# Kernel tuning notes

Measured on AMD Instinct MI355X. Metric: run time of the kernel, lower is better.

The kernel has to match this reference:

```python
import jax, jax.numpy as jnp
import numpy as np
from jax import lax

VOCAB = 50000
EMB = 300
HID = 256
N = 4096          # total_sents
T_COL = 64
T_ROW = 16
N_DOCS = 512


def setup_inputs() -> dict:
    key = jax.random.key(0)
    ks = jax.random.split(key, 20)

    def glorot(k, shape):
        fan = float(sum(shape))
        return (jax.random.normal(k, shape, jnp.float32) * (2.0 / fan) ** 0.5)

    inp = {}
    inp["col"] = jax.random.randint(ks[0], (N, T_COL), 0, VOCAB, dtype=jnp.int32)
    inp["row"] = jax.random.randint(ks[1], (N, T_ROW), 0, VOCAB, dtype=jnp.int32)
    inp["row_neg"] = jax.random.randint(ks[2], (N, T_ROW), 0, VOCAB, dtype=jnp.int32)
    # pack_padded_sequence expects lengths sorted descending
    inp["col_lens"] = jnp.sort(jax.random.randint(ks[3], (N,), 1, T_COL + 1, dtype=jnp.int32))[::-1]
    inp["row_lens"] = jnp.sort(jax.random.randint(ks[4], (N,), 1, T_ROW + 1, dtype=jnp.int32))[::-1]
    inp["row_neg_lens"] = jnp.sort(jax.random.randint(ks[5], (N,), 1, T_ROW + 1, dtype=jnp.int32))[::-1]
    inp["col_refs"] = jax.random.randint(ks[6], (N,), 0, N_DOCS, dtype=jnp.int32)
    inp["row_refs"] = jax.random.randint(ks[7], (N,), 0, N_DOCS, dtype=jnp.int32)
    inp["row_neg_refs"] = jax.random.randint(ks[8], (N,), 0, N_DOCS, dtype=jnp.int32)
    inp["embed_table"] = jax.random.normal(ks[9], (VOCAB, EMB), jnp.float32) * 0.1
    inp["col_W_ih"] = glorot(ks[10], (4 * HID, EMB))
    inp["col_W_hh"] = glorot(ks[11], (4 * HID, HID))
    inp["col_b_ih"] = jnp.zeros((4 * HID,), jnp.float32)
    inp["col_b_hh"] = jnp.zeros((4 * HID,), jnp.float32)
    inp["row_W_ih"] = glorot(ks[12], (4 * HID, EMB))
    inp["row_W_hh"] = glorot(ks[13], (4 * HID, HID))
    inp["row_b_ih"] = jnp.zeros((4 * HID,), jnp.float32)
    inp["row_b_hh"] = jnp.zeros((4 * HID,), jnp.float32)
    return inp


def lstm_last_hidden(x, lengths, W_ih, W_hh, b_ih, b_hh):
    """x: [N,T,E]; returns hidden state at step lengths-1 per sequence: [N,H].
    Equivalent to torch LSTM over a packed padded sequence (state frozen past len)."""
    Nn, T, _ = x.shape
    H = W_hh.shape[1]
    h0 = jnp.zeros((Nn, H), x.dtype)
    bias = b_ih + b_hh

    def step(carry, inputs):
        h, c = carry
        xt, t = inputs  # xt: [N,E]
        gates = xt @ W_ih.T + h @ W_hh.T + bias  # [N,4H]
        i, f, g, o = jnp.split(gates, 4, axis=-1)  # torch gate order i,f,g,o
        i = jax.nn.sigmoid(i); f = jax.nn.sigmoid(f); o = jax.nn.sigmoid(o)
        g = jnp.tanh(g)
        c_new = f * c + i * g
        h_new = o * jnp.tanh(c_new)
        m = (t < lengths)[:, None]
        return (jnp.where(m, h_new, h), jnp.where(m, c_new, c)), None

    (h, _), _ = lax.scan(step, (h0, h0), (jnp.swapaxes(x, 0, 1), jnp.arange(T)))
    return h


def reference(col, row, row_neg, col_lens, row_lens, row_neg_lens,
              col_refs, row_refs, row_neg_refs, embed_table,
              col_W_ih, col_W_hh, col_b_ih, col_b_hh,
              row_W_ih, row_W_hh, row_b_ih, row_b_hh):
    # Dropout is identity (eval-mode reference).
    def compose(tokens, lens, refs, W_ih, W_hh, b_ih, b_hh):
        emb = embed_table[tokens]                      # [N,T,E]
        h = lstm_last_hidden(emb, lens, W_ih, W_hh, b_ih, b_hh)  # [N,H]
        # mask-multiply + sum == segment-sum of hidden states by doc ref,
        # scattered into a [total_sents, H] buffer (rows >= n_docs are zero)
        return jax.ops.segment_sum(h, refs, num_segments=tokens.shape[0])

    col_h = compose(col, col_lens, col_refs, col_W_ih, col_W_hh, col_b_ih, col_b_hh)
    row_h = compose(row, row_lens, row_refs, row_W_ih, row_W_hh, row_b_ih, row_b_hh)
    neg_h = compose(row_neg, row_neg_lens, row_neg_refs, row_W_ih, row_W_hh, row_b_ih, row_b_hh)

    pos = jnp.sum(col_h * row_h, axis=1)
    neg = jnp.sum(col_h * neg_h, axis=1)
    # BPRLoss(size_average=False): sum of -logsigmoid(pos - neg)
    return -jnp.sum(jax.nn.log_sigmoid(pos - neg))
```

## Files before the change

kernel.cpp:

```cpp
#include <hip/hip_runtime.h>


typedef __bf16 bf16x8 __attribute__((ext_vector_type(8)));
typedef float  fvec4  __attribute__((ext_vector_type(4)));

#define NSEN 4096
#define HIDN 256
#define EMBD 300
#define VOC  50000

#define OFF_P     0ULL
#define OFF_BPK   204800000ULL
#define OFF_WHHC  206110720ULL
#define OFF_WHHR  206635008ULL
#define OFF_BIAS  207159296ULL
#define OFF_SEG   219750400ULL
#define OFF_LOSS  232333312ULL

static __device__ __forceinline__ unsigned short f2bf(float x) {
    unsigned int u = __float_as_uint(x);
    unsigned int r = (u + 0x7fffu + ((u >> 16) & 1u)) >> 16;
    return (unsigned short)r;
}
static __device__ __forceinline__ float bf2f(unsigned short b) {
    return __uint_as_float(((unsigned int)b) << 16);
}
static __device__ __forceinline__ float sigm(float x) { return 1.f / (1.f + __expf(-x)); }
static __device__ __forceinline__ float tanh_(float x) {
    float e = __expf(2.f * x);
    return 1.f - 2.f / (e + 1.f);
}
static __device__ __forceinline__ fvec4 unpk(uint2 v) {
    fvec4 o;
    o[0] = __uint_as_float((v.x & 0xffffu) << 16);
    o[1] = __uint_as_float(v.x & 0xffff0000u);
    o[2] = __uint_as_float((v.y & 0xffffu) << 16);
    o[3] = __uint_as_float(v.y & 0xffff0000u);
    return o;
}

static __device__ __forceinline__ void gld_lds16(const unsigned short* g,
                                                 unsigned short* l)
{
    __builtin_amdgcn_global_load_lds(
        (const __attribute__((address_space(1))) unsigned int*)g,
        (__attribute__((address_space(3))) unsigned int*)l, 16, 0, 0);
}

static __device__ __forceinline__ int whh_src(int o) {
    int L  = o >> 9;
    int r9 = o & 511;
    int ln = r9 >> 3, j = r9 & 7;
    int g  = L & 3, kt = (L >> 2) & 7, wv = (L >> 5) & 15;
    int row = g * 256 + wv * 16 + (ln & 15);
    int col = kt * 32 + (ln >> 4) * 8 + j;
    return row * 256 + col;
}

__global__ void prep_kernel(
    const float* __restrict__ cWih, const float* __restrict__ rWih,
    const float* __restrict__ cWhh, const float* __restrict__ rWhh,
    const float* __restrict__ cbih, const float* __restrict__ cbhh,
    const float* __restrict__ rbih, const float* __restrict__ rbhh,
    unsigned short* __restrict__ Bpk, unsigned short* __restrict__ WhhC,
    unsigned short* __restrict__ WhhR, float* __restrict__ biascat)
{
    int idx = blockIdx.x * 256 + threadIdx.x;
    if (idx < 655360) {
        int e = idx & 511, lnn = e >> 3, j = e & 7;
        int f = idx >> 9;
        int ntt = f & 3;
        int kc = f >> 2;
        int kt = kc % 10;
        int s  = kc / 10;
        int n = (s >> 1) * 128 + (s & 1) * 64 + ntt * 16 + (lnn & 15);
        int k = kt * 32 + (lnn >> 4) * 8 + j;
        float v = 0.f;
        if (k < EMBD) v = (n < 1024) ? cWih[n * EMBD + k] : rWih[(n - 1024) * EMBD + k];
        Bpk[idx] = f2bf(v);
        return;
    }
    idx -= 655360;
    if (idx < 262144) { WhhC[idx] = f2bf(cWhh[whh_src(idx)]); return; }
    idx -= 262144;
    if (idx < 262144) { WhhR[idx] = f2bf(rWhh[whh_src(idx)]); return; }
    idx -= 262144;
    if (idx < 2048)
        biascat[idx] = (idx < 1024) ? (cbih[idx] + cbhh[idx])
                                    : (rbih[idx - 1024] + rbhh[idx - 1024]);
}

__global__ __launch_bounds__(256) void gemm_p_kernel(
    const float* __restrict__ A,
    const unsigned short* __restrict__ Bpk,
    const float* __restrict__ bias,
    unsigned short* __restrict__ Pout)
{
    const int mb = blockIdx.x * 128;
    const int tid = threadIdx.x;
    const int wv = tid >> 6, ln = tid & 63, l15 = ln & 15, q = ln >> 4;
    const int wm = wv & 1, wn = wv >> 1;

    __shared__ __align__(16) unsigned short At[2][4][10][512];

    {
        int row = tid >> 1, kh = tid & 1;
        int gr = mb + row;
        unsigned short* dst = &At[row >> 6][(row >> 4) & 3][0][0];
        const int fl = row & 15;
        #pragma unroll
        for (int i = 0; i < 40; ++i) {
            int k = kh * 160 + i * 4;
            float4 v = make_float4(0.f, 0.f, 0.f, 0.f);
            if (gr < VOC && k < EMBD)
                v = *(const float4*)(A + (size_t)gr * EMBD + k);
            ushort4 b;
            b.x = f2bf(v.x); b.y = f2bf(v.y); b.z = f2bf(v.z); b.w = f2bf(v.w);
            int di = (k >> 5) * 512 + ((k >> 3) & 3) * 128 + fl * 8 + (k & 7);
            *(ushort4*)(dst + di) = b;
        }
    }
    __syncthreads();

    for (int nc = 0; nc < 16; ++nc) {
        fvec4 acc[4][4];
        #pragma unroll
        for (int a = 0; a < 4; ++a)
            #pragma unroll
            for (int b = 0; b < 4; ++b) acc[a][b] = (fvec4)0.f;

        #pragma unroll 2
        for (int kt = 0; kt < 10; ++kt) {
            const unsigned short* bp =
                Bpk + (size_t)(((nc * 2 + wn) * 10 + kt) * 4) * 512 + ln * 8;
            bf16x8 bfr[4];
            #pragma unroll
            for (int ntt = 0; ntt < 4; ++ntt)
                bfr[ntt] = *(const bf16x8*)(bp + ntt * 512);
            #pragma unroll
            for (int mt = 0; mt < 4; ++mt) {
                bf16x8 af = *(const bf16x8*)&At[wm][mt][kt][ln * 8];
                #pragma unroll
                for (int ntt = 0; ntt < 4; ++ntt)
                    acc[mt][ntt] = __builtin_amdgcn_mfma_f32_16x16x32_bf16(
                        af, bfr[ntt], acc[mt][ntt], 0, 0, 0);
            }
        }
        float bv[4];
        #pragma unroll
        for (int ntt = 0; ntt < 4; ++ntt)
            bv[ntt] = bias[nc * 128 + wn * 64 + ntt * 16 + l15];
        #pragma unroll
        for (int mt = 0; mt < 4; ++mt) {
            #pragma unroll
            for (int r = 0; r < 4; ++r) {
                int m = mb + wm * 64 + mt * 16 + q * 4 + r;
                if (m < VOC) {
                    size_t base = (size_t)m * 2048 + nc * 128 + wn * 64;
                    #pragma unroll
                    for (int ntt = 0; ntt < 4; ++ntt)
                        Pout[base + ntt * 16 + l15] = f2bf(acc[mt][ntt][r] + bv[ntt]);
                }
            }
        }
    }
}

__global__ __launch_bounds__(1024, 2) void lstm_kernel(
    const int* __restrict__ colTok, const int* __restrict__ rowTok, const int* __restrict__ negTok,
    const int* __restrict__ colLen, const int* __restrict__ rowLen, const int* __restrict__ negLen,
    const int* __restrict__ crefs, const int* __restrict__ rrefs, const int* __restrict__ nrefs,
    const unsigned short* __restrict__ P,
    const unsigned short* __restrict__ WhhC, const unsigned short* __restrict__ WhhR,
    float* __restrict__ seg)
{
    const int part = blockIdx.x >> 8;
    const int sb = blockIdx.x & 255;
    const int s0 = sb * 16;
    const int* tok = part == 0 ? colTok : (part == 1 ? rowTok : negTok);
    const int* len = part == 0 ? colLen : (part == 1 ? rowLen : negLen);
    const int* refs = part == 0 ? crefs : (part == 1 ? rrefs : nrefs);
    const unsigned short* Whh = part == 0 ? WhhC : WhhR;
    const int T = part == 0 ? 64 : 16;
    const int pco = part == 0 ? 0 : 1024;
    float* segp = seg + (size_t)part * 1048576;

    const int tid = threadIdx.x;
    const int wv = tid >> 6;
    const int ln = tid & 63, l15 = ln & 15, q = ln >> 4;

    __shared__ __align__(16) unsigned short hx[2][8][4][16][8];
    __shared__ __align__(16) unsigned short pstage[2][16][4][2][16][8];
    __shared__ __align__(16) char ldspad[1536];
    char* hB0 = (char*)&hx[0][0][0][0][0];
    char* hB1 = (char*)&hx[1][0][0][0][0];

    for (int i = tid; i < 8192; i += 1024) (&hx[0][0][0][0][0])[i] = 0;

    const int len0 = len[s0 + l15];
    int ml = len0;
    #pragma unroll
    for (int off = 1; off < 16; off <<= 1) ml = max(ml, __shfl_xor(ml, off));
    const int maxlen = ml;
    if (maxlen < 0) ldspad[tid & 1023] = 1;

    const unsigned short* wbase = Whh + (size_t)wv * 16384 + (size_t)ln * 8;

    const int wrByte = (wv >> 1) * 1024 + ((wv & 1) * 2 + (q >> 1)) * 256 +
                       l15 * 16 + (q & 1) * 8;

    const int dg = ln >> 5, dh = (ln >> 4) & 1;

    float c[4];
    #pragma unroll
    for (int r = 0; r < 4; ++r) c[r] = 0.f;
    ushort4 hpk = make_ushort4(0, 0, 0, 0);

    __syncthreads();

    {
        int tk = tok[(s0 + l15) * T];
        #pragma unroll
        for (int d = 0; d < 2; ++d) {
            const unsigned short* src = P + (size_t)tk * 2048 + pco +
                (2 * d + dg) * 256 + wv * 16 + dh * 8;
            gld_lds16(src, &pstage[0][wv][2 * d][0][0][0]);
        }
    }
    int tknext = tok[(s0 + l15) * T + 1];

    for (int t = 0; t < maxlen; ++t) {
        const int pb = t & 1;
        const char* hRd = (t & 1) ? hB1 : hB0;
        char* hWr = (t & 1) ? hB0 : hB1;

        asm volatile("s_waitcnt vmcnt(0)" ::: "memory");

        fvec4 acc[4];
        #pragma unroll
        for (int g = 0; g < 4; ++g)
            acc[g] = unpk(*(const uint2*)
                &pstage[pb][wv][g][q >> 1][l15][(q & 1) * 4]);

        #pragma unroll 2
        for (int kt = 0; kt < 8; ++kt) {
            bf16x8 b0 = *(const bf16x8*)(hRd + kt * 1024 + ln * 16);
            #pragma unroll
            for (int g = 0; g < 4; ++g) {
                bf16x8 a = *(const bf16x8*)(wbase + (size_t)(kt * 4 + g) * 512);
                acc[g] = __builtin_amdgcn_mfma_f32_16x16x32_bf16(a, b0, acc[g], 0, 0, 0);
            }
        }

        if (t + 1 < maxlen) {
            __builtin_amdgcn_sched_barrier(0);
            #pragma unroll
            for (int d = 0; d < 2; ++d) {
                const unsigned short* src = P + (size_t)tknext * 2048 + pco +
                    (2 * d + dg) * 256 + wv * 16 + dh * 8;
                gld_lds16(src, &pstage[pb ^ 1][wv][2 * d][0][0][0]);
            }
            int t2 = (t + 2 < T) ? (t + 2) : (T - 1);
            tknext = tok[(s0 + l15) * T + t2];
        }

        {
            bool act = t < len0;
            if (act) {
                float hr[4];
                #pragma unroll
                for (int r = 0; r < 4; ++r) {
                    float iv = acc[0][r];
                    float fv = acc[1][r];
                    float gv = acc[2][r];
                    float ov = acc[3][r];
                    float cn = sigm(fv) * c[r] + sigm(iv) * tanh_(gv);
                    c[r] = cn;
                    hr[r] = sigm(ov) * tanh_(cn);
                }
                hpk = make_ushort4(f2bf(hr[0]), f2bf(hr[1]),
                                   f2bf(hr[2]), f2bf(hr[3]));
            }
            *(ushort4*)(hWr + wrByte) = hpk;
        }
        asm volatile("s_waitcnt lgkmcnt(0)\n\ts_barrier" ::: "memory");
    }

    const char* hF = (maxlen & 1) ? hB1 : hB0;
    for (int i = tid; i < 16 * HIDN; i += 1024) {
        int sq = i >> 8, hd = i & 255;
        unsigned short hv = *(const unsigned short*)
            (hF + (hd >> 5) * 1024 + ((hd >> 3) & 3) * 256 +
             sq * 16 + (hd & 7) * 2);
        int rf = refs[s0 + sq];
        atomicAdd(segp + (size_t)rf * 256 + hd, bf2f(hv));
    }
}

__global__ void loss_kernel(const float* __restrict__ seg, float* __restrict__ part)
{
    int d = blockIdx.x, tid = threadIdx.x;
    const float* sc = seg + (size_t)d * 256;
    const float* sr = seg + 1048576 + (size_t)d * 256;
    const float* sn = seg + 2097152 + (size_t)d * 256;
    float a = sc[tid];
    float p = a * sr[tid];
    float n = a * sn[tid];
    for (int off = 32; off; off >>= 1) { p += __shfl_down(p, off); n += __shfl_down(n, off); }
    __shared__ float rp[4], rn[4];
    if ((tid & 63) == 0) { rp[tid >> 6] = p; rn[tid >> 6] = n; }
    __syncthreads();
    if (tid == 0) {
        float Ps = rp[0] + rp[1] + rp[2] + rp[3];
        float Ns = rn[0] + rn[1] + rn[2] + rn[3];
        float x = Ps - Ns;
        part[d] = fmaxf(-x, 0.f) + log1pf(expf(-fabsf(x)));
    }
}

__global__ void reduce_kernel(const float* __restrict__ part, float* __restrict__ out)
{
    int tid = threadIdx.x;
    float s = 0.f;
    for (int i = tid; i < 4096; i += 256) s += part[i];
    for (int off = 32; off; off >>= 1) s += __shfl_down(s, off);
    __shared__ float r[4];
    if ((tid & 63) == 0) r[tid >> 6] = s;
    __syncthreads();
    if (tid == 0) out[0] = r[0] + r[1] + r[2] + r[3];
}

extern "C" void kernel_launch(void* const* d_in, const int* in_sizes, int n_in,
                              void* d_out, int out_size, void* d_ws, size_t ws_size,
                              hipStream_t stream)
{
    const int*   col      = (const int*)d_in[0];
    const int*   row      = (const int*)d_in[1];
    const int*   rneg     = (const int*)d_in[2];
    const int*   col_lens = (const int*)d_in[3];
    const int*   row_lens = (const int*)d_in[4];
    const int*   rng_lens = (const int*)d_in[5];
    const int*   col_refs = (const int*)d_in[6];
    const int*   row_refs = (const int*)d_in[7];
    const int*   rng_refs = (const int*)d_in[8];
    const float* embed    = (const float*)d_in[9];
    const float* cWih     = (const float*)d_in[10];
    const float* cWhh     = (const float*)d_in[11];
    const float* cbih     = (const float*)d_in[12];
    const float* cbhh     = (const float*)d_in[13];
    const float* rWih     = (const float*)d_in[14];
    const float* rWhh     = (const float*)d_in[15];
    const float* rbih     = (const float*)d_in[16];
    const float* rbhh     = (const float*)d_in[17];

    char* ws = (char*)d_ws;
    unsigned short* P    = (unsigned short*)(ws + OFF_P);
    unsigned short* Bpk  = (unsigned short*)(ws + OFF_BPK);
    unsigned short* WhhC = (unsigned short*)(ws + OFF_WHHC);
    unsigned short* WhhR = (unsigned short*)(ws + OFF_WHHR);
    float* biascat = (float*)(ws + OFF_BIAS);
    float* seg     = (float*)(ws + OFF_SEG);
    float* lpart   = (float*)(ws + OFF_LOSS);

    hipMemsetAsync(seg, 0, 3 * 4096 * 256 * sizeof(float), stream);

    prep_kernel<<<4616, 256, 0, stream>>>(cWih, rWih, cWhh, rWhh,
                                          cbih, cbhh, rbih, rbhh,
                                          Bpk, WhhC, WhhR, biascat);
    gemm_p_kernel<<<391, 256, 0, stream>>>(embed, Bpk, biascat, P);
    lstm_kernel<<<768, 1024, 0, stream>>>(col, row, rneg,
                                          col_lens, row_lens, rng_lens,
                                          col_refs, row_refs, rng_refs,
                                          P, WhhC, WhhR, seg);
    loss_kernel<<<4096, 256, 0, stream>>>(seg, lpart);
    reduce_kernel<<<1, 256, 0, stream>>>(lpart, (float*)d_out);
}
```

Baseline: 689.5 us.

## Keep half of W_hh in registers and single-buffer the input projection stage

Half of each wave's recurrent weight fragments (the first four k-tiles) are now loaded once into registers instead of being re-read from global memory every timestep. The staging buffer for precomputed input projections goes from double to single buffering, and the padding array that forced an LDS size limit is removed. The projection add moves after the MFMA loop, with a wait on the prefetch placed there, so the global load latency overlaps the matmul. This lowers per-step weight traffic and LDS use, which may allow more blocks per CU. The cost is 64 extra VGPRs per thread and a serialized prefetch within each step.

Result: faster. 601.4 us (-12.8%).

```diff
diff --git a/kernel.cpp b/kernel.cpp
--- a/kernel.cpp
+++ b/kernel.cpp
@@ -190,8 +190,7 @@
     const int ln = tid & 63, l15 = ln & 15, q = ln >> 4;
 
     __shared__ __align__(16) unsigned short hx[2][8][4][16][8];
-    __shared__ __align__(16) unsigned short pstage[2][16][4][2][16][8];
-    __shared__ __align__(16) char ldspad[1536];
+    __shared__ __align__(16) unsigned short pstage[16][4][2][16][8];
     char* hB0 = (char*)&hx[0][0][0][0][0];
     char* hB1 = (char*)&hx[1][0][0][0][0];
 
@@ -202,7 +201,6 @@
     #pragma unroll
     for (int off = 1; off < 16; off <<= 1) ml = max(ml, __shfl_xor(ml, off));
     const int maxlen = ml;
-    if (maxlen < 0) ldspad[tid & 1023] = 1;
 
     const unsigned short* wbase = Whh + (size_t)wv * 16384 + (size_t)ln * 8;
 
@@ -216,6 +214,13 @@
     for (int r = 0; r < 4; ++r) c[r] = 0.f;
     ushort4 hpk = make_ushort4(0, 0, 0, 0);
 
+    bf16x8 wres[4][4];
+    #pragma unroll
+    for (int kt = 0; kt < 4; ++kt)
+        #pragma unroll
+        for (int g = 0; g < 4; ++g)
+            wres[kt][g] = *(const bf16x8*)(wbase + (size_t)(kt * 4 + g) * 512);
+
     __syncthreads();
 
     {
@@ -224,26 +229,29 @@
         for (int d = 0; d < 2; ++d) {
             const unsigned short* src = P + (size_t)tk * 2048 + pco +
                 (2 * d + dg) * 256 + wv * 16 + dh * 8;
-            gld_lds16(src, &pstage[0][wv][2 * d][0][0][0]);
+            gld_lds16(src, &pstage[wv][2 * d][0][0][0]);
         }
     }
     int tknext = tok[(s0 + l15) * T + 1];
 
     for (int t = 0; t < maxlen; ++t) {
-        const int pb = t & 1;
         const char* hRd = (t & 1) ? hB1 : hB0;
         char* hWr = (t & 1) ? hB0 : hB1;
 
-        asm volatile("s_waitcnt vmcnt(0)" ::: "memory");
-
         fvec4 acc[4];
         #pragma unroll
-        for (int g = 0; g < 4; ++g)
-            acc[g] = unpk(*(const uint2*)
-                &pstage[pb][wv][g][q >> 1][l15][(q & 1) * 4]);
-
+        for (int g = 0; g < 4; ++g) acc[g] = (fvec4)0.f;
+
+        #pragma unroll
+        for (int kt = 0; kt < 4; ++kt) {
+            bf16x8 b0 = *(const bf16x8*)(hRd + kt * 1024 + ln * 16);
+            #pragma unroll
+            for (int g = 0; g < 4; ++g)
+                acc[g] = __builtin_amdgcn_mfma_f32_16x16x32_bf16(
+                    wres[kt][g], b0, acc[g], 0, 0, 0);
+        }
         #pragma unroll 2
-        for (int kt = 0; kt < 8; ++kt) {
+        for (int kt = 4; kt < 8; ++kt) {
             bf16x8 b0 = *(const bf16x8*)(hRd + kt * 1024 + ln * 16);
             #pragma unroll
             for (int g = 0; g < 4; ++g) {
@@ -252,13 +260,22 @@
             }
         }
 
+        asm volatile("s_waitcnt vmcnt(0)" ::: "memory");
+        #pragma unroll
+        for (int g = 0; g < 4; ++g) {
+            fvec4 pv = unpk(*(const uint2*)
+                &pstage[wv][g][q >> 1][l15][(q & 1) * 4]);
+            acc[g] += pv;
+        }
+
         if (t + 1 < maxlen) {
+            asm volatile("s_waitcnt lgkmcnt(0)" ::: "memory");
             __builtin_amdgcn_sched_barrier(0);
             #pragma unroll
             for (int d = 0; d < 2; ++d) {
                 const unsigned short* src = P + (size_t)tknext * 2048 + pco +
                     (2 * d + dg) * 256 + wv * 16 + dh * 8;
-                gld_lds16(src, &pstage[pb ^ 1][wv][2 * d][0][0][0]);
+                gld_lds16(src, &pstage[wv][2 * d][0][0][0]);
             }
             int t2 = (t + 2 < T) ? (t + 2) : (T - 1);
             tknext = tok[(s0 + l15) * T + t2];
```
